# Kernel optimization log

Measured on AMD Instinct MI355X. Metric: run time of the kernel, lower is better.

The kernel has to match this reference:

```python
import jax, jax.numpy as jnp
import numpy as np

EPS = 1e-6

def setup_inputs() -> dict:
    key = jax.random.key(0)
    ks = jax.random.split(key, 9)
    B, D, F = 8192, 2048, 1024
    s_in = 1.0 / np.sqrt(D)
    return {
        "Q": jax.random.normal(ks[0], (B, D), jnp.float32),
        "K": jax.random.normal(ks[1], (B, D), jnp.float32),
        "V": jax.random.normal(ks[2], (B, D), jnp.float32),
        "Wq": jax.random.normal(ks[3], (D, F), jnp.float32) * s_in,
        "bq": jnp.zeros((F,), jnp.float32),
        "Wk": jax.random.normal(ks[4], (D, F), jnp.float32) * s_in,
        "bk": jnp.zeros((F,), jnp.float32),
        "Wv": jax.random.normal(ks[5], (D, D), jnp.float32) * s_in,
        "bv": jnp.zeros((D,), jnp.float32),
    }

def reference(Q, K, V, Wq, bq, Wk, bk, Wv, bv):
    # feature maps: Linear + ELU (note: ELU, no +1, matching the source)
    Q_feat = jax.nn.elu(Q @ Wq + bq)          # (B, F)
    K_feat = jax.nn.elu(K @ Wk + bk)          # (B, F)
    V_proj = V @ Wv + bv                      # (B, D)
    # torch: KV = outer(K_feat, V_proj); QKV = Q_feat @ KV
    # equivalent without materializing (B, F, D):
    qk = jnp.einsum('bi,bi->b', Q_feat, K_feat)      # (B,)
    QKV = qk[:, None] * V_proj                        # (B, D)
    # Z = 1 / (sum_i Q_feat * sum_i K_feat + eps)
    Z = 1.0 / (Q_feat.sum(-1) * K_feat.sum(-1) + EPS)  # (B,)
    return QKV * Z[:, None]
```

## Files before the change

kernel.cpp:

```cpp
#include <hip/hip_runtime.h>
#include <hip/hip_fp16.h>
#include <cstdint>
#include <cstddef>

typedef _Float16 f16x8 __attribute__((ext_vector_type(8)));
typedef _Float16 f16x4 __attribute__((ext_vector_type(4)));
typedef float    f32x4 __attribute__((ext_vector_type(4)));

#define GPTR(p) ((const __attribute__((address_space(1))) void*)(p))
#define SPTR(p) ((__attribute__((address_space(3))) void*)(p))

__global__ void transpose_cast_kernel(const float* __restrict__ W,
                                      _Float16* __restrict__ Wt,
                                      int R, int C) {
  __shared__ float tile[32][33];
  const int c  = blockIdx.x * 32 + threadIdx.x;
  const int r0 = blockIdx.y * 32;
  for (int i = threadIdx.y; i < 32; i += 8)
    tile[i][threadIdx.x] = W[(size_t)(r0 + i) * C + c];
  __syncthreads();
  const int out_c = r0 + threadIdx.x;
  const int oc0   = blockIdx.x * 32;
  for (int i = threadIdx.y; i < 32; i += 8)
    Wt[(size_t)(oc0 + i) * R + out_c] = (_Float16)tile[threadIdx.x][i];
}

__global__ void cast_f32_f16_kernel(const float* __restrict__ src,
                                    _Float16* __restrict__ dst) {
  const size_t i = (size_t)blockIdx.x * 256 + threadIdx.x;
  const float4 v = ((const float4*)src)[i];
  f16x4 h;
  h[0] = (_Float16)v.x; h[1] = (_Float16)v.y;
  h[2] = (_Float16)v.z; h[3] = (_Float16)v.w;
  ((f16x4*)dst)[i] = h;
}

template <int MODE, bool AHALF, bool OUTHALF>
__global__ __launch_bounds__(256) void gemm2(
    const void* __restrict__ Av,
    const _Float16* __restrict__ Bt0, const _Float16* __restrict__ Bt1,
    const float* __restrict__ bias0, const float* __restrict__ bias1,
    int msplit, const float* __restrict__ scale,
    void* __restrict__ Cv, int K, int N) {
  constexpr int BK = 64;
  __shared__ __align__(16) _Float16 As[128 * BK];
  __shared__ __align__(16) _Float16 Bs[128 * BK];

  const int tid  = threadIdx.x;
  const int lane = tid & 63;
  const int wave = tid >> 6;
  const int quad = lane >> 4;
  const int r    = lane & 15;
  const int wm   = wave >> 1;
  const int wn   = wave & 1;
  const int m0   = blockIdx.y * 128;
  const int n0   = blockIdx.x * 128;

  const _Float16* Bt  = (m0 >= msplit) ? Bt1 : Bt0;
  const float* bias   = (m0 >= msplit) ? bias1 : bias0;

  size_t aoff[4], boff[4];
  int slot[4];
#pragma unroll
  for (int t = 0; t < 4; ++t) {
    const int s  = wave * 256 + t * 64 + lane;
    const int n  = s >> 3;
    const int kc = (s & 7) ^ (n & 7);
    aoff[t] = (size_t)(m0 + n) * K + kc * 8;
    boff[t] = (size_t)(n0 + n) * K + kc * 8;
    slot[t] = s;
  }

  f32x4 acc[4][4] = {};
  const _Float16* Ah = (const _Float16*)Av;
  const float*    Af = (const float*)Av;

  for (int k0 = 0; k0 < K; k0 += BK) {
    __syncthreads();
    if (AHALF) {
#pragma unroll
      for (int t = 0; t < 4; ++t)
        __builtin_amdgcn_global_load_lds(GPTR(Ah + aoff[t] + k0),
                                         SPTR(As + (wave * 256 + t * 64) * 8),
                                         16, 0, 0);
    } else {
#pragma unroll
      for (int t = 0; t < 4; ++t) {
        const float* ap = Af + aoff[t] + k0;
        const float4 v0 = *(const float4*)ap;
        const float4 v1 = *(const float4*)(ap + 4);
        f16x8 h;
        h[0] = (_Float16)v0.x; h[1] = (_Float16)v0.y;
        h[2] = (_Float16)v0.z; h[3] = (_Float16)v0.w;
        h[4] = (_Float16)v1.x; h[5] = (_Float16)v1.y;
        h[6] = (_Float16)v1.z; h[7] = (_Float16)v1.w;
        *(f16x8*)(As + (size_t)slot[t] * 8) = h;
      }
    }
#pragma unroll
    for (int t = 0; t < 4; ++t)
      __builtin_amdgcn_global_load_lds(GPTR(Bt + boff[t] + k0),
                                       SPTR(Bs + (wave * 256 + t * 64) * 8),
                                       16, 0, 0);
    __syncthreads();

#pragma unroll
    for (int ki = 0; ki < 2; ++ki) {
      f16x8 af[4], bf[4];
#pragma unroll
      for (int i = 0; i < 4; ++i) {
        const int an = wm * 64 + i * 16 + r;
        af[i] = *(const f16x8*)(As + (an * 8 + ((ki * 4 + quad) ^ (an & 7))) * 8);
      }
#pragma unroll
      for (int j = 0; j < 4; ++j) {
        const int bn = wn * 64 + j * 16 + r;
        bf[j] = *(const f16x8*)(Bs + (bn * 8 + ((ki * 4 + quad) ^ (bn & 7))) * 8);
      }
#pragma unroll
      for (int i = 0; i < 4; ++i)
#pragma unroll
        for (int j = 0; j < 4; ++j)
          acc[i][j] = __builtin_amdgcn_mfma_f32_16x16x32_f16(af[i], bf[j],
                                                             acc[i][j], 0, 0, 0);
    }
  }

  float*    Cf = (float*)Cv;
  _Float16* Ch = (_Float16*)Cv;
#pragma unroll
  for (int i = 0; i < 4; ++i) {
#pragma unroll
    for (int j = 0; j < 4; ++j) {
      const int col = n0 + wn * 64 + j * 16 + r;
      const float b = bias[col];
#pragma unroll
      for (int reg = 0; reg < 4; ++reg) {
        const int row = m0 + wm * 64 + i * 16 + quad * 4 + reg;
        float v = acc[i][j][reg] + b;
        if (MODE == 0) v = v > 0.f ? v : (expf(v) - 1.f);
        else           v = v * scale[row];
        if (OUTHALF) Ch[(size_t)row * N + col] = (_Float16)v;
        else         Cf[(size_t)row * N + col] = v;
      }
    }
  }
}

template <bool HALF>
__global__ void reduce_scale2(const void* __restrict__ Qf,
                              const void* __restrict__ Kf,
                              float* __restrict__ scale) {
  const int b = blockIdx.x;
  const int t = threadIdx.x;
  float q[4], k[4];
  if (HALF) {
    const f16x4 qh = ((const f16x4*)((const _Float16*)Qf + (size_t)b * 1024))[t];
    const f16x4 kh = ((const f16x4*)((const _Float16*)Kf + (size_t)b * 1024))[t];
#pragma unroll
    for (int i = 0; i < 4; ++i) { q[i] = (float)qh[i]; k[i] = (float)kh[i]; }
  } else {
    const float4 qv = ((const float4*)((const float*)Qf + (size_t)b * 1024))[t];
    const float4 kv = ((const float4*)((const float*)Kf + (size_t)b * 1024))[t];
    q[0] = qv.x; q[1] = qv.y; q[2] = qv.z; q[3] = qv.w;
    k[0] = kv.x; k[1] = kv.y; k[2] = kv.z; k[3] = kv.w;
  }
  float qk = q[0] * k[0] + q[1] * k[1] + q[2] * k[2] + q[3] * k[3];
  float sq = q[0] + q[1] + q[2] + q[3];
  float sk = k[0] + k[1] + k[2] + k[3];
#pragma unroll
  for (int off = 32; off > 0; off >>= 1) {
    qk += __shfl_down(qk, off, 64);
    sq += __shfl_down(sq, off, 64);
    sk += __shfl_down(sk, off, 64);
  }
  __shared__ float buf[3][4];
  const int lane = t & 63, wv = t >> 6;
  if (lane == 0) { buf[0][wv] = qk; buf[1][wv] = sq; buf[2][wv] = sk; }
  __syncthreads();
  if (t == 0) {
    const float QK = buf[0][0] + buf[0][1] + buf[0][2] + buf[0][3];
    const float SQ = buf[1][0] + buf[1][1] + buf[1][2] + buf[1][3];
    const float SK = buf[2][0] + buf[2][1] + buf[2][2] + buf[2][3];
    scale[b] = QK / (SQ * SK + 1e-6f);
  }
}

extern "C" void kernel_launch(void* const* d_in, const int* in_sizes, int n_in,
                              void* d_out, int out_size, void* d_ws,
                              size_t ws_size, hipStream_t stream) {
  const float* Q  = (const float*)d_in[0];
  const float* K_ = (const float*)d_in[1];
  const float* V  = (const float*)d_in[2];
  const float* Wq = (const float*)d_in[3];
  const float* bq = (const float*)d_in[4];
  const float* Wk = (const float*)d_in[5];
  const float* bk = (const float*)d_in[6];
  const float* Wv = (const float*)d_in[7];
  const float* bv = (const float*)d_in[8];
  float* out = (float*)d_out;

  const int B = 8192, D = 2048, F = 1024;
  const size_t MiB = 1u << 20;
  char* ws = (char*)d_ws;

  const size_t NEED_FAST = 40 * MiB + 64 * 1024;

  if (ws_size >= NEED_FAST) {
    _Float16* WqT = (_Float16*)ws;
    _Float16* WkT = (_Float16*)(ws + 4 * MiB);
    _Float16* WvT = (_Float16*)ws;
    _Float16* QfH = (_Float16*)(ws + 8 * MiB);
    _Float16* KfH = (_Float16*)(ws + 24 * MiB);
    _Float16* Vh  = (_Float16*)(ws + 8 * MiB);
    float* scale  = (float*)(ws + 40 * MiB);
    _Float16* Qh = (_Float16*)d_out;
    _Float16* Kh = (_Float16*)d_out + (size_t)B * D;

    dim3 tb(32, 8);
    transpose_cast_kernel<<<dim3(F / 32, D / 32), tb, 0, stream>>>(Wq, WqT, D, F);
    transpose_cast_kernel<<<dim3(F / 32, D / 32), tb, 0, stream>>>(Wk, WkT, D, F);
    const int castBlocks = (B * D / 4) / 256;
    cast_f32_f16_kernel<<<castBlocks, 256, 0, stream>>>(Q,  Qh);
    cast_f32_f16_kernel<<<castBlocks, 256, 0, stream>>>(K_, Kh);

    gemm2<0, true, true><<<dim3(F / 128, (2 * B) / 128), 256, 0, stream>>>(
        Qh, WqT, WkT, bq, bk, B, nullptr, QfH, D, F);
    reduce_scale2<true><<<B, 256, 0, stream>>>(QfH, KfH, scale);

    cast_f32_f16_kernel<<<castBlocks, 256, 0, stream>>>(V, Vh);
    transpose_cast_kernel<<<dim3(D / 32, D / 32), tb, 0, stream>>>(Wv, WvT, D, D);
    gemm2<1, true, false><<<dim3(D / 128, B / 128), 256, 0, stream>>>(
        Vh, WvT, WvT, bv, bv, 1 << 30, scale, out, D, D);
  } else {
    _Float16* WqT = (_Float16*)ws;
    _Float16* WkT = (_Float16*)(ws + 4 * MiB);
    _Float16* WvT = (_Float16*)(ws + 8 * MiB);
    float* scale  = (float*)(ws + 16 * MiB);
    float* Qf = out;
    float* Kf = out + (size_t)B * F;

    dim3 tb(32, 8);
    transpose_cast_kernel<<<dim3(F / 32, D / 32), tb, 0, stream>>>(Wq, WqT, D, F);
    transpose_cast_kernel<<<dim3(F / 32, D / 32), tb, 0, stream>>>(Wk, WkT, D, F);
    transpose_cast_kernel<<<dim3(D / 32, D / 32), tb, 0, stream>>>(Wv, WvT, D, D);

    gemm2<0, false, false><<<dim3(F / 128, B / 128), 256, 0, stream>>>(
        Q, WqT, WqT, bq, bq, 1 << 30, nullptr, Qf, D, F);
    gemm2<0, false, false><<<dim3(F / 128, B / 128), 256, 0, stream>>>(
        K_, WkT, WkT, bk, bk, 1 << 30, nullptr, Kf, D, F);
    reduce_scale2<false><<<B, 256, 0, stream>>>(Qf, Kf, scale);
    gemm2<1, false, false><<<dim3(D / 128, B / 128), 256, 0, stream>>>(
        V, WvT, WvT, bv, bv, 1 << 30, scale, out, D, D);
  }
}
```

Before: 439.5 us.

## Add 256x256-tile triple-buffered GEMM with direct global-to-LDS loads

```diff
diff --git a/kernel.cpp b/kernel.cpp
--- a/kernel.cpp
+++ b/kernel.cpp
@@ -35,6 +35,131 @@
   ((f16x4*)dst)[i] = h;
 }
 
+#define STAGE256(Asw, Bsw, kk) do {                                            \
+    _Pragma("unroll")                                                          \
+    for (int rep_ = 0; rep_ < 2; ++rep_)                                       \
+      __builtin_amdgcn_global_load_lds(GPTR(asrc[rep_] + (kk)),                \
+                                       SPTR((Asw) + ldst[rep_]), 16, 0, 0);    \
+    _Pragma("unroll")                                                          \
+    for (int rep_ = 0; rep_ < 2; ++rep_)                                       \
+      __builtin_amdgcn_global_load_lds(GPTR(bsrc[rep_] + (kk)),                \
+                                       SPTR((Bsw) + ldst[rep_]), 16, 0, 0);    \
+  } while (0)
+
+#define COMPUTE256(Asr, Bsr) do {                                              \
+    f16x8 af[8], bf[4];                                                        \
+    _Pragma("unroll")                                                          \
+    for (int i_ = 0; i_ < 8; ++i_) {                                           \
+      const int an_ = wm * 128 + i_ * 16 + r;                                  \
+      const int ap_ = an_ >> 1;                                                \
+      const int sl_ = ap_ * 8 + ((((an_ & 1) << 2) | quad) ^ (ap_ & 7));       \
+      af[i_] = *(const f16x8*)((Asr) + sl_ * 8);                               \
+    }                                                                          \
+    _Pragma("unroll")                                                          \
+    for (int j_ = 0; j_ < 4; ++j_) {                                           \
+      const int bn_ = wn * 64 + j_ * 16 + r;                                   \
+      const int bp_ = bn_ >> 1;                                                \
+      const int sl_ = bp_ * 8 + ((((bn_ & 1) << 2) | quad) ^ (bp_ & 7));       \
+      bf[j_] = *(const f16x8*)((Bsr) + sl_ * 8);                               \
+    }                                                                          \
+    __builtin_amdgcn_s_setprio(1);                                             \
+    _Pragma("unroll")                                                          \
+    for (int i_ = 0; i_ < 8; ++i_)                                             \
+      _Pragma("unroll")                                                        \
+      for (int j_ = 0; j_ < 4; ++j_)                                           \
+        acc[i_][j_] = __builtin_amdgcn_mfma_f32_16x16x32_f16(af[i_], bf[j_],   \
+                                                             acc[i_][j_],      \
+                                                             0, 0, 0);         \
+    __builtin_amdgcn_s_setprio(0);                                             \
+  } while (0)
+
+template <int MODE, bool OUTHALF>
+__global__ __launch_bounds__(512, 2) void gemm256(
+    const _Float16* __restrict__ A,
+    const _Float16* __restrict__ Bt0, const _Float16* __restrict__ Bt1,
+    const float* __restrict__ bias0, const float* __restrict__ bias1,
+    int msplit, const float* __restrict__ scale,
+    void* __restrict__ Cv, int K, int N) {
+  __shared__ __align__(16) _Float16 As0[8192], As1[8192], As2[8192];
+  __shared__ __align__(16) _Float16 Bs0[8192], Bs1[8192], Bs2[8192];
+
+  const int tid  = threadIdx.x;
+  const int lane = tid & 63;
+  const int wave = tid >> 6;
+  const int quad = lane >> 4;
+  const int r    = lane & 15;
+  const int wm   = wave >> 2;
+  const int wn   = wave & 3;
+
+  const int gx  = gridDim.x;
+  const int nwg = gx * gridDim.y;
+  int flat = blockIdx.y * gx + blockIdx.x;
+  if ((nwg & 7) == 0) flat = (flat & 7) * (nwg >> 3) + (flat >> 3);
+  const int m0 = (flat / gx) * 256;
+  const int n0 = (flat % gx) * 256;
+
+  const _Float16* Bt  = (m0 >= msplit) ? Bt1 : Bt0;
+  const float*    bias = (m0 >= msplit) ? bias1 : bias0;
+
+  const _Float16* asrc[2];
+  const _Float16* bsrc[2];
+  int ldst[2];
+#pragma unroll
+  for (int rep = 0; rep < 2; ++rep) {
+    const int s   = rep * 512 + tid;
+    const int p   = s >> 3;
+    const int sub = (s & 7) ^ (p & 7);
+    const int row = p * 2 + (sub >> 2);
+    const int kc  = sub & 3;
+    asrc[rep] = A  + (size_t)(m0 + row) * K + kc * 8;
+    bsrc[rep] = Bt + (size_t)(n0 + row) * K + kc * 8;
+    ldst[rep] = (rep * 512 + wave * 64) * 8;
+  }
+
+  f32x4 acc[8][4] = {};
+  const int NT = K >> 5;
+
+  STAGE256(As0, Bs0, 0);
+  STAGE256(As1, Bs1, 32);
+
+  for (int t = 0; t < NT; ++t) {
+    if (t + 1 < NT) asm volatile("s_waitcnt vmcnt(4)" ::: "memory");
+    else            asm volatile("s_waitcnt vmcnt(0)" ::: "memory");
+    __builtin_amdgcn_s_barrier();
+    asm volatile("" ::: "memory");
+    const int k2 = (t + 2) << 5;
+    switch (t % 3) {
+      case 0: if (t + 2 < NT) STAGE256(As2, Bs2, k2); COMPUTE256(As0, Bs0); break;
+      case 1: if (t + 2 < NT) STAGE256(As0, Bs0, k2); COMPUTE256(As1, Bs1); break;
+      default:if (t + 2 < NT) STAGE256(As1, Bs1, k2); COMPUTE256(As2, Bs2); break;
+    }
+  }
+
+  float*    Cf = (float*)Cv;
+  _Float16* Ch = (_Float16*)Cv;
+#pragma unroll
+  for (int i = 0; i < 8; ++i) {
+    const int row0 = m0 + wm * 128 + i * 16 + quad * 4;
+#pragma unroll
+    for (int j = 0; j < 4; ++j) {
+      const int col = n0 + wn * 64 + j * 16 + r;
+      const float b = bias[col];
+#pragma unroll
+      for (int reg = 0; reg < 4; ++reg) {
+        const int row = row0 + reg;
+        float v = acc[i][j][reg] + b;
+        if (MODE == 0) v = v > 0.f ? v : (expf(v) - 1.f);
+        else           v = v * scale[row];
+        if (OUTHALF) Ch[(size_t)row * N + col] = (_Float16)v;
+        else         Cf[(size_t)row * N + col] = v;
+      }
+    }
+  }
+}
+
+#undef STAGE256
+#undef COMPUTE256
+
 template <int MODE, bool AHALF, bool OUTHALF>
 __global__ __launch_bounds__(256) void gemm2(
     const void* __restrict__ Av,
@@ -224,13 +349,13 @@
     cast_f32_f16_kernel<<<castBlocks, 256, 0, stream>>>(Q,  Qh);
     cast_f32_f16_kernel<<<castBlocks, 256, 0, stream>>>(K_, Kh);
 
-    gemm2<0, true, true><<<dim3(F / 128, (2 * B) / 128), 256, 0, stream>>>(
+    gemm256<0, true><<<dim3(F / 256, (2 * B) / 256), 512, 0, stream>>>(
         Qh, WqT, WkT, bq, bk, B, nullptr, QfH, D, F);
     reduce_scale2<true><<<B, 256, 0, stream>>>(QfH, KfH, scale);
 
     cast_f32_f16_kernel<<<castBlocks, 256, 0, stream>>>(V, Vh);
     transpose_cast_kernel<<<dim3(D / 32, D / 32), tb, 0, stream>>>(Wv, WvT, D, D);
-    gemm2<1, true, false><<<dim3(D / 128, B / 128), 256, 0, stream>>>(
+    gemm256<1, false><<<dim3(D / 256, B / 256), 512, 0, stream>>>(
         Vh, WvT, WvT, bv, bv, 1 << 30, scale, out, D, D);
   } else {
     _Float16* WqT = (_Float16*)ws;
```

Result: slower. 849.1 us (+93.2%).
